# Optimization experiments

Hardware: AMD Instinct MI355X
Metric: run time of the kernel (lower is better)

Reference implementation:

```python
import jax, jax.numpy as jnp
import numpy as np

B, H, S, D = 4, 16, 2048, 64


def setup_inputs() -> dict:
    key = jax.random.key(0)
    kq, kk, kv = jax.random.split(key, 3)
    Q = jax.random.normal(kq, (B, H, S, D), dtype=jnp.float32)
    K = jax.random.normal(kk, (B, H, S, D), dtype=jnp.float32)
    V = jax.random.normal(kv, (B, H, S, D), dtype=jnp.float32)
    # causal mask, broadcasts over (B, H); True = keep, False (==0) = mask out
    mask = jnp.tril(jnp.ones((S, S), dtype=bool))
    return {"Q": Q, "K": K, "V": V, "mask": mask}


def reference(Q, K, V, mask):
    d_k = Q.shape[-1]
    scale = 1.0 / jnp.sqrt(jnp.asarray(d_k, dtype=Q.dtype))
    # [B,H,Sq,Sk] score matrix (the module materializes this fully)
    scores = jnp.einsum('bhqd,bhkd->bhqk', Q, K) * scale
    if mask is not None:
        scores = jnp.where(mask, scores, -jnp.inf)
    attn = jax.nn.softmax(scores, axis=-1)
    return jnp.einsum('bhqk,bhkd->bhqd', attn, V)
```

## Files before the change

kernel.cpp:

```cpp
#include <hip/hip_runtime.h>
#include <math.h>

namespace {

constexpr int SEQ   = 2048;
constexpr int DH    = 64;
constexpr int KVBLK = 64;
constexpr int BH    = 64;
constexpr size_t WS_NEED = (size_t)BH * SEQ * DH * 2  * 2 ;

typedef __bf16 bf16x8 __attribute__((ext_vector_type(8)));
typedef float  f32x16 __attribute__((ext_vector_type(16)));

union FragB { bf16x8 v; unsigned u[4]; };

__device__ __forceinline__ unsigned pack2(float a, float b) {
  unsigned r;
  asm("v_cvt_pk_bf16_f32 %0, %1, %2" : "=v"(r) : "v"(a), "v"(b));
  return r;
}

__device__ __forceinline__ unsigned short bf16c(float f) {
  union { float f; unsigned u; } v; v.f = f;
  unsigned r = v.u + 0x7fffu + ((v.u >> 16) & 1u);
  return (unsigned short)(r >> 16);
}

__device__ __forceinline__ void swap32(int a, int b, int &x, int &y) {
#if __has_builtin(__builtin_amdgcn_permlane32_swap)
  auto r = __builtin_amdgcn_permlane32_swap(a, b, false, false);
  x = r[0]; y = r[1];
#else
  const bool hi = ((threadIdx.x & 63) >= 32);
  const int sa = __shfl_xor(a, 32), sb = __shfl_xor(b, 32);
  x = hi ? sb : a;
  y = hi ? b  : sa;
#endif
}

__device__ __forceinline__ float xhalf_sum(float v) {
  int x, y; swap32(__float_as_int(v), __float_as_int(v), x, y);
  return __int_as_float(x) + __int_as_float(y);
}

__device__ __forceinline__ void gload16(const void* g, void* l) {
  __builtin_amdgcn_global_load_lds(
      (const __attribute__((address_space(1))) void*)g,
      (__attribute__((address_space(3))) void*)l, 16, 0, 0);
}

__global__ __launch_bounds__(256)
void prep(const float* __restrict__ Kg, const float* __restrict__ Vg,
          unsigned short* __restrict__ wsK, unsigned short* __restrict__ wsV)
{
  const int blk = blockIdx.x;
  const int bh  = blk & 63;
  const int t   = blk >> 6;
  const int tid = threadIdx.x;

  const float* Kb = Kg + (size_t)bh * SEQ * DH;
  unsigned short* wK = wsK + (size_t)bh * SEQ * DH;
#pragma unroll
  for (int i = 0; i < 2; ++i) {
    const int kc  = tid + i * 256;
    const int row = kc >> 3, c = kc & 7;
    const int csrc = c ^ (row & 7);
    const float* s = Kb + (size_t)(t*64 + row) * DH + csrc * 8;
    float4 a = *(const float4*)s, b2 = *(const float4*)(s + 4);
    uint4 w;
    w.x = pack2(a.x, a.y);   w.y = pack2(a.z, a.w);
    w.z = pack2(b2.x, b2.y); w.w = pack2(b2.z, b2.w);
    *(uint4*)&wK[(size_t)(t*64 + row) * DH + c * 8] = w;
  }

  __shared__ unsigned short vt[64 * 64];
  const float* Vb = Vg + (size_t)bh * SEQ * DH;
  {
    const int kv = tid >> 2;
    const int d0 = (tid & 3) * 16;
    const float* s = Vb + (size_t)(t*64 + kv) * DH + d0;
#pragma unroll
    for (int e = 0; e < 16; ++e) {
      const int d = d0 + e;
      const int slot = (kv >> 3) ^ (d & 7);
      vt[d*64 + slot*8 + (kv & 7)] = bf16c(s[e]);
    }
  }
  __syncthreads();
  unsigned short* wV = wsV + (size_t)bh * SEQ * DH + (size_t)t * 4096;
#pragma unroll
  for (int i = 0; i < 2; ++i) {
    const int o = (tid + i * 256) * 8;
    *(uint4*)&wV[o] = *(const uint4*)&vt[o];
  }
}

__global__ __launch_bounds__(256, 2)
void attn_fwd(const float* __restrict__ Qg, const unsigned short* __restrict__ wsK,
              const unsigned short* __restrict__ wsV, float* __restrict__ Og)
{
  const int b   = blockIdx.x;
  const int bh  = b & 63;
  const int qi  = 31 - (b >> 6);
  const int NT  = qi + 1;

  const int tid  = threadIdx.x;
  const int wv   = tid >> 6;
  const int rw   = wv & 1;
  const int kh   = wv >> 1;
  const int lane = tid & 63;
  const int l31  = lane & 31;
  const int hi   = lane >> 5;
  const int qloc = rw * 32 + l31;

  const float* Qp = Qg + (size_t)bh * SEQ * DH;
  const unsigned short* Kw = wsK + (size_t)bh * SEQ * DH;
  const unsigned short* Vw = wsV + (size_t)bh * SEQ * DH;
  float* Op = Og + (size_t)bh * SEQ * DH;

  __shared__ __align__(16) unsigned char smem[32768];

  const float qscale = 0.125f * 1.44269504088896f;
  FragB bq[4];
  {
    const float* src = Qp + (size_t)(qi*64 + rw*32 + l31) * DH + hi*8;
#pragma unroll
    for (int ks = 0; ks < 4; ++ks) {
      float4 f0 = *(const float4*)(src + ks*16);
      float4 f1 = *(const float4*)(src + ks*16 + 4);
      bq[ks].u[0] = pack2(f0.x*qscale, f0.y*qscale);
      bq[ks].u[1] = pack2(f0.z*qscale, f0.w*qscale);
      bq[ks].u[2] = pack2(f1.x*qscale, f1.y*qscale);
      bq[ks].u[3] = pack2(f1.z*qscale, f1.w*qscale);
    }
  }

  f32x16 oacc[2];
#pragma unroll
  for (int dt = 0; dt < 2; ++dt)
#pragma unroll
    for (int r = 0; r < 16; ++r) oacc[dt][r] = 0.f;
  float lpart = 0.f;

  auto stage = [&](int tile, int bufoff) {
    const unsigned short* gK = Kw + (size_t)tile * 4096 + wv*512 + lane*8;
    const unsigned short* gV = Vw + (size_t)tile * 4096 + wv*512 + lane*8;
    char* lb = (char*)smem + bufoff + wv*1024;
    gload16(gK,        lb);
    gload16(gK + 2048, lb + 4096);
    gload16(gV,        lb + 8192);
    gload16(gV + 2048, lb + 12288);
  };

  auto compute = [&](bool diag, int bufoff) {
    const unsigned short* Kl = (const unsigned short*)(smem + bufoff);
    const unsigned short* Vl = (const unsigned short*)(smem + bufoff + 8192);
    const int krow = kh*32 + l31;

    f32x16 st;
#pragma unroll
    for (int r = 0; r < 16; ++r) st[r] = 0.f;
    __builtin_amdgcn_s_setprio(1);
#pragma unroll
    for (int ks = 0; ks < 4; ++ks) {
      bf16x8 ak = *(const bf16x8*)&Kl[krow*64 + (((2*ks + hi) ^ (krow & 7)) * 8)];
      st = __builtin_amdgcn_mfma_f32_32x32x16_bf16(ak, bq[ks].v, st, 0, 0, 0);
    }
    __builtin_amdgcn_s_setprio(0);

    float p[16];
#pragma unroll
    for (int r = 0; r < 16; ++r) {
      float s = st[r];
      if (diag) {
        const int kvl = kh*32 + (r & 3) + 4*hi + 8*(r >> 2);
        if (kvl > qloc) s = -INFINITY;
      }
      const float e = exp2f(s);
      p[r] = e;
      lpart += e;
    }

    unsigned pk[8];
#pragma unroll
    for (int j2 = 0; j2 < 8; ++j2) pk[j2] = pack2(p[2*j2], p[2*j2 + 1]);

    FragB pa[2];
#pragma unroll
    for (int ks2 = 0; ks2 < 2; ++ks2) {
      const int gA = 2*ks2, gB = 2*ks2 + 1;
      int x0, y0, x1, y1;
      swap32((int)pk[2*gA],     (int)pk[2*gB],     x0, y0);
      swap32((int)pk[2*gA + 1], (int)pk[2*gB + 1], x1, y1);
      pa[ks2].u[0] = (unsigned)x0;
      pa[ks2].u[1] = (unsigned)x1;
      pa[ks2].u[2] = (unsigned)y0;
      pa[ks2].u[3] = (unsigned)y1;
    }

    __builtin_amdgcn_s_setprio(1);
#pragma unroll
    for (int dt = 0; dt < 2; ++dt) {
      const int d = dt*32 + l31;
#pragma unroll
      for (int ks2 = 0; ks2 < 2; ++ks2) {
        bf16x8 av = *(const bf16x8*)&Vl[d*64 + (((4*kh + 2*ks2 + hi) ^ (d & 7)) * 8)];
        oacc[dt] = __builtin_amdgcn_mfma_f32_32x32x16_bf16(av, pa[ks2].v, oacc[dt], 0, 0, 0);
      }
    }
    __builtin_amdgcn_s_setprio(0);
  };

  stage(0, 0);
  __syncthreads();

  for (int t = 0; t < NT; t += 2) {
    if (t + 1 < NT) stage(t + 1, 16384);
    compute(t == NT - 1, 0);
    __syncthreads();
    if (t + 1 < NT) {
      if (t + 2 < NT) stage(t + 2, 0);
      compute(t + 1 == NT - 1, 16384);
      __syncthreads();
    }
  }

  {
    float* reg0 = reinterpret_cast<float*>(smem);
    float* reg1 = reinterpret_cast<float*>(smem + 16384);
    float* myreg = rw ? reg1 : reg0;
    const int rb = l31 * 68;

    if (kh == 1) {
#pragma unroll
      for (int dt = 0; dt < 2; ++dt)
#pragma unroll
        for (int g4 = 0; g4 < 4; ++g4) {
          float4 w;
          w.x = oacc[dt][4*g4 + 0]; w.y = oacc[dt][4*g4 + 1];
          w.z = oacc[dt][4*g4 + 2]; w.w = oacc[dt][4*g4 + 3];
          *(float4*)&myreg[rb + dt*32 + 8*g4 + 4*hi] = w;
        }
      const float s1 = xhalf_sum(lpart);
      if (hi == 0) myreg[rb + 64] = s1;
    }
    __syncthreads();
    if (kh == 0) {
      const float linv = 1.0f / (xhalf_sum(lpart) + myreg[rb + 64]);
#pragma unroll
      for (int dt = 0; dt < 2; ++dt)
#pragma unroll
        for (int g4 = 0; g4 < 4; ++g4) {
          float4 v = *(const float4*)&myreg[rb + dt*32 + 8*g4 + 4*hi];
          v.x = (v.x + oacc[dt][4*g4 + 0]) * linv;
          v.y = (v.y + oacc[dt][4*g4 + 1]) * linv;
          v.z = (v.z + oacc[dt][4*g4 + 2]) * linv;
          v.w = (v.w + oacc[dt][4*g4 + 3]) * linv;
          *(float4*)&myreg[rb + dt*32 + 8*g4 + 4*hi] = v;
        }
    }
    __syncthreads();
    {
      float* dst = Op + (size_t)(qi * 64) * DH;
#pragma unroll
      for (int i = 0; i < 4; ++i) {
        const int f   = tid + i*256;
        const int row = f >> 4;
        const int ch  = f & 15;
        const float* srcrow = (row < 32) ? (reg0 + row*68) : (reg1 + (row-32)*68);
        float4 v = *(const float4*)&srcrow[ch*4];
        *(float4*)&dst[(size_t)row*DH + ch*4] = v;
      }
    }
  }
}

constexpr int PADB = 72;

__global__ __launch_bounds__(256, 2)
void attn_fb(const float* __restrict__ Qg, const float* __restrict__ Kg,
             const float* __restrict__ Vg, float* __restrict__ Og)
{
  const int b   = blockIdx.x;
  const int bh  = b & 63;
  const int qi  = 31 - (b >> 6);
  const int NT  = qi + 1;
  const int tid  = threadIdx.x;
  const int wv   = tid >> 6;
  const int rw   = wv & 1;
  const int kh   = wv >> 1;
  const int lane = tid & 63;
  const int l31  = lane & 31;
  const int hi   = lane >> 5;
  const int qloc = rw * 32 + l31;

  const size_t base = (size_t)bh * SEQ * DH;
  const float* Qp = Qg + base;
  const float* Kp = Kg + base;
  const float* Vp = Vg + base;
  float*       Op = Og + base;

  __shared__ __align__(16) unsigned char smem[18432];
  auto K_lds  = reinterpret_cast<__bf16(*)[PADB]>(smem);
  auto Vt_lds = reinterpret_cast<__bf16(*)[PADB]>(smem + 9216);

  const float qscale = 0.125f * 1.44269504088896f;
  FragB bq[4];
  {
    const float* src = Qp + (size_t)(qi*64 + rw*32 + l31) * DH + hi*8;
#pragma unroll
    for (int ks = 0; ks < 4; ++ks) {
      float4 f0 = *(const float4*)(src + ks*16);
      float4 f1 = *(const float4*)(src + ks*16 + 4);
      bq[ks].u[0] = pack2(f0.x*qscale, f0.y*qscale);
      bq[ks].u[1] = pack2(f0.z*qscale, f0.w*qscale);
      bq[ks].u[2] = pack2(f1.x*qscale, f1.y*qscale);
      bq[ks].u[3] = pack2(f1.z*qscale, f1.w*qscale);
    }
  }

  float4 kr[2][2];
  float  vr[16];
  const int kc8 = tid & 7;
  const int vd  = tid & 63;
  const int vk0 = (tid >> 6) * 16;

  auto load_tile = [&](int tile) {
    const int kvb = tile * KVBLK;
#pragma unroll
    for (int p = 0; p < 2; ++p) {
      const float* s = Kp + (size_t)(kvb + 32*p + (tid >> 3)) * DH + kc8*8;
      kr[p][0] = *(const float4*)s;
      kr[p][1] = *(const float4*)(s + 4);
    }
#pragma unroll
    for (int r = 0; r < 16; ++r)
      vr[r] = Vp[(size_t)(kvb + vk0 + r) * DH + vd];
  };

  auto store_tile = [&]() {
#pragma unroll
    for (int p = 0; p < 2; ++p) {
      uint4 w;
      w.x = pack2(kr[p][0].x, kr[p][0].y); w.y = pack2(kr[p][0].z, kr[p][0].w);
      w.z = pack2(kr[p][1].x, kr[p][1].y); w.w = pack2(kr[p][1].z, kr[p][1].w);
      *reinterpret_cast<uint4*>(&K_lds[32*p + (tid >> 3)][kc8*8]) = w;
    }
    uint4 w0, w1;
    w0.x = pack2(vr[0],  vr[1]);  w0.y = pack2(vr[2],  vr[3]);
    w0.z = pack2(vr[4],  vr[5]);  w0.w = pack2(vr[6],  vr[7]);
    w1.x = pack2(vr[8],  vr[9]);  w1.y = pack2(vr[10], vr[11]);
    w1.z = pack2(vr[12], vr[13]); w1.w = pack2(vr[14], vr[15]);
    *reinterpret_cast<uint4*>(&Vt_lds[vd][vk0])     = w0;
    *reinterpret_cast<uint4*>(&Vt_lds[vd][vk0 + 8]) = w1;
  };

  f32x16 oacc[2];
#pragma unroll
  for (int dt = 0; dt < 2; ++dt)
#pragma unroll
    for (int r = 0; r < 16; ++r) oacc[dt][r] = 0.f;
  float lpart = 0.f;

  load_tile(0);
  store_tile();
  __syncthreads();

  for (int t = 0; t < NT; ++t) {
    if (t + 1 < NT) load_tile(t + 1);
    const bool diag = (t == NT - 1);

    f32x16 st;
#pragma unroll
    for (int r = 0; r < 16; ++r) st[r] = 0.f;
#pragma unroll
    for (int ks = 0; ks < 4; ++ks) {
      bf16x8 ak = *(const bf16x8*)&K_lds[kh*32 + l31][ks*16 + hi*8];
      st = __builtin_amdgcn_mfma_f32_32x32x16_bf16(ak, bq[ks].v, st, 0, 0, 0);
    }

    float p[16];
#pragma unroll
    for (int r = 0; r < 16; ++r) {
      float s = st[r];
      if (diag) {
        const int kvl = kh*32 + (r & 3) + 4*hi + 8*(r >> 2);
        if (kvl > qloc) s = -INFINITY;
      }
      const float e = exp2f(s);
      p[r] = e;
      lpart += e;
    }

    unsigned pk[8];
#pragma unroll
    for (int j2 = 0; j2 < 8; ++j2) pk[j2] = pack2(p[2*j2], p[2*j2 + 1]);

    FragB pa[2];
#pragma unroll
    for (int ks2 = 0; ks2 < 2; ++ks2) {
      const int gA = 2*ks2, gB = 2*ks2 + 1;
      int x0, y0, x1, y1;
      swap32((int)pk[2*gA],     (int)pk[2*gB],     x0, y0);
      swap32((int)pk[2*gA + 1], (int)pk[2*gB + 1], x1, y1);
      pa[ks2].u[0] = (unsigned)x0;
      pa[ks2].u[1] = (unsigned)x1;
      pa[ks2].u[2] = (unsigned)y0;
      pa[ks2].u[3] = (unsigned)y1;
    }

#pragma unroll
    for (int dt = 0; dt < 2; ++dt)
#pragma unroll
      for (int ks2 = 0; ks2 < 2; ++ks2) {
        bf16x8 av = *(const bf16x8*)&Vt_lds[dt*32 + l31][kh*32 + ks2*16 + hi*8];
        oacc[dt] = __builtin_amdgcn_mfma_f32_32x32x16_bf16(av, pa[ks2].v, oacc[dt], 0, 0, 0);
      }

    __syncthreads();
    if (t + 1 < NT) {
      store_tile();
      __syncthreads();
    }
  }

  {
    float* reg0 = reinterpret_cast<float*>(smem);
    float* reg1 = reinterpret_cast<float*>(smem + 9216);
    float* myreg = rw ? reg1 : reg0;
    const int rb = l31 * 68;

    if (kh == 1) {
#pragma unroll
      for (int dt = 0; dt < 2; ++dt)
#pragma unroll
        for (int g4 = 0; g4 < 4; ++g4) {
          float4 w;
          w.x = oacc[dt][4*g4 + 0]; w.y = oacc[dt][4*g4 + 1];
          w.z = oacc[dt][4*g4 + 2]; w.w = oacc[dt][4*g4 + 3];
          *(float4*)&myreg[rb + dt*32 + 8*g4 + 4*hi] = w;
        }
      const float s1 = xhalf_sum(lpart);
      if (hi == 0) myreg[rb + 64] = s1;
    }
    __syncthreads();
    if (kh == 0) {
      const float linv = 1.0f / (xhalf_sum(lpart) + myreg[rb + 64]);
#pragma unroll
      for (int dt = 0; dt < 2; ++dt)
#pragma unroll
        for (int g4 = 0; g4 < 4; ++g4) {
          float4 v = *(const float4*)&myreg[rb + dt*32 + 8*g4 + 4*hi];
          v.x = (v.x + oacc[dt][4*g4 + 0]) * linv;
          v.y = (v.y + oacc[dt][4*g4 + 1]) * linv;
          v.z = (v.z + oacc[dt][4*g4 + 2]) * linv;
          v.w = (v.w + oacc[dt][4*g4 + 3]) * linv;
          *(float4*)&myreg[rb + dt*32 + 8*g4 + 4*hi] = v;
        }
    }
    __syncthreads();
    {
      float* dst = Op + (size_t)(qi * 64) * DH;
#pragma unroll
      for (int i = 0; i < 4; ++i) {
        const int f   = tid + i*256;
        const int row = f >> 4;
        const int ch  = f & 15;
        const float* srcrow = (row < 32) ? (reg0 + row*68) : (reg1 + (row-32)*68);
        float4 v = *(const float4*)&srcrow[ch*4];
        *(float4*)&dst[(size_t)row*DH + ch*4] = v;
      }
    }
  }
}

}

extern "C" void kernel_launch(void* const* d_in, const int* in_sizes, int n_in,
                              void* d_out, int out_size, void* d_ws, size_t ws_size,
                              hipStream_t stream) {
  const float* Q = (const float*)d_in[0];
  const float* K = (const float*)d_in[1];
  const float* V = (const float*)d_in[2];
  float* O = (float*)d_out;
  if (ws_size >= WS_NEED) {
    unsigned short* wsK = (unsigned short*)d_ws;
    unsigned short* wsV = wsK + (size_t)BH * SEQ * DH;
    prep<<<dim3(BH * 32), dim3(256), 0, stream>>>(K, V, wsK, wsV);
    attn_fwd<<<dim3(32 * BH), dim3(256), 0, stream>>>(Q, wsK, wsV, O);
  } else {
    attn_fb<<<dim3(32 * BH), dim3(256), 0, stream>>>(Q, K, V, O);
  }
}
```

Before: 81.23 us.

## Process 128-query tiles with 8 waves sharing each staged K/V tile

The attention kernel now uses 512-thread blocks that each handle 128 query rows, so every K/V tile staged into LDS is reused by four row-waves instead of two, halving the grid and the per-block global-to-LDS traffic per query. Waves covering the lower half of the query tile skip compute on the final KV tile they do not need. The epilogue reduces the two KV-half partial accumulators in two rounds and writes output directly from registers rather than through an LDS staging copy. The cost is larger blocks, with idle waves on the last tile and extra barriers, and direct global stores that may coalesce less well.

```diff
diff --git a/kernel.cpp b/kernel.cpp
--- a/kernel.cpp
+++ b/kernel.cpp
@@ -95,23 +95,24 @@
   }
 }
 
-__global__ __launch_bounds__(256, 2)
+__global__ __launch_bounds__(512, 4)
 void attn_fwd(const float* __restrict__ Qg, const unsigned short* __restrict__ wsK,
               const unsigned short* __restrict__ wsV, float* __restrict__ Og)
 {
   const int b   = blockIdx.x;
   const int bh  = b & 63;
-  const int qi  = 31 - (b >> 6);
-  const int NT  = qi + 1;
+  const int qi  = 15 - (b >> 6);
+  const int NT  = 2 * qi + 2;
 
   const int tid  = threadIdx.x;
   const int wv   = tid >> 6;
-  const int rw   = wv & 1;
-  const int kh   = wv >> 1;
+  const int rw   = wv & 3;
+  const int kh   = wv >> 2;
   const int lane = tid & 63;
   const int l31  = lane & 31;
   const int hi   = lane >> 5;
-  const int qloc = rw * 32 + l31;
+  const int qrel = (rw & 1) * 32 + l31;
+  const int tmaxw = 2*qi + (rw >> 1);
 
   const float* Qp = Qg + (size_t)bh * SEQ * DH;
   const unsigned short* Kw = wsK + (size_t)bh * SEQ * DH;
@@ -123,7 +124,7 @@
   const float qscale = 0.125f * 1.44269504088896f;
   FragB bq[4];
   {
-    const float* src = Qp + (size_t)(qi*64 + rw*32 + l31) * DH + hi*8;
+    const float* src = Qp + (size_t)(qi*128 + rw*32 + l31) * DH + hi*8;
 #pragma unroll
     for (int ks = 0; ks < 4; ++ks) {
       float4 f0 = *(const float4*)(src + ks*16);
@@ -146,10 +147,8 @@
     const unsigned short* gK = Kw + (size_t)tile * 4096 + wv*512 + lane*8;
     const unsigned short* gV = Vw + (size_t)tile * 4096 + wv*512 + lane*8;
     char* lb = (char*)smem + bufoff + wv*1024;
-    gload16(gK,        lb);
-    gload16(gK + 2048, lb + 4096);
-    gload16(gV,        lb + 8192);
-    gload16(gV + 2048, lb + 12288);
+    gload16(gK, lb);
+    gload16(gV, lb + 8192);
   };
 
   auto compute = [&](bool diag, int bufoff) {
@@ -174,7 +173,7 @@
       float s = st[r];
       if (diag) {
         const int kvl = kh*32 + (r & 3) + 4*hi + 8*(r >> 2);
-        if (kvl > qloc) s = -INFINITY;
+        if (kvl > qrel) s = -INFINITY;
       }
       const float e = exp2f(s);
       p[r] = e;
@@ -216,22 +215,22 @@
 
   for (int t = 0; t < NT; t += 2) {
     if (t + 1 < NT) stage(t + 1, 16384);
-    compute(t == NT - 1, 0);
+    if (t <= tmaxw) compute(t == tmaxw, 0);
     __syncthreads();
     if (t + 1 < NT) {
       if (t + 2 < NT) stage(t + 2, 0);
-      compute(t + 1 == NT - 1, 16384);
+      if (t + 1 <= tmaxw) compute(t + 1 == tmaxw, 16384);
       __syncthreads();
     }
   }
 
-  {
-    float* reg0 = reinterpret_cast<float*>(smem);
-    float* reg1 = reinterpret_cast<float*>(smem + 16384);
-    float* myreg = rw ? reg1 : reg0;
-    const int rb = l31 * 68;
-
-    if (kh == 1) {
+  const int qrow = qi*128 + rw*32 + l31;
+#pragma unroll
+  for (int round = 0; round < 2; ++round) {
+    __syncthreads();
+    if ((rw >> 1) == round && kh == 1) {
+      float* reg = reinterpret_cast<float*>(smem) + (rw & 1) * 4096;
+      const int rb = l31 * 65;
 #pragma unroll
       for (int dt = 0; dt < 2; ++dt)
 #pragma unroll
@@ -239,38 +238,28 @@
           float4 w;
           w.x = oacc[dt][4*g4 + 0]; w.y = oacc[dt][4*g4 + 1];
           w.z = oacc[dt][4*g4 + 2]; w.w = oacc[dt][4*g4 + 3];
-          *(float4*)&myreg[rb + dt*32 + 8*g4 + 4*hi] = w;
+          *(float4*)&reg[rb + dt*32 + 8*g4 + 4*hi] = w;
         }
       const float s1 = xhalf_sum(lpart);
-      if (hi == 0) myreg[rb + 64] = s1;
-    }
-    __syncthreads();
-    if (kh == 0) {
-      const float linv = 1.0f / (xhalf_sum(lpart) + myreg[rb + 64]);
+      if (hi == 0) reg[rb + 64] = s1;
+    }
+    __syncthreads();
+    if ((rw >> 1) == round && kh == 0) {
+      const float* reg = reinterpret_cast<const float*>(smem) + (rw & 1) * 4096;
+      const int rb = l31 * 65;
+      const float linv = 1.0f / (xhalf_sum(lpart) + reg[rb + 64]);
+      float* dst = Op + (size_t)qrow * DH;
 #pragma unroll
       for (int dt = 0; dt < 2; ++dt)
 #pragma unroll
         for (int g4 = 0; g4 < 4; ++g4) {
-          float4 v = *(const float4*)&myreg[rb + dt*32 + 8*g4 + 4*hi];
+          float4 v = *(const float4*)&reg[rb + dt*32 + 8*g4 + 4*hi];
           v.x = (v.x + oacc[dt][4*g4 + 0]) * linv;
           v.y = (v.y + oacc[dt][4*g4 + 1]) * linv;
           v.z = (v.z + oacc[dt][4*g4 + 2]) * linv;
           v.w = (v.w + oacc[dt][4*g4 + 3]) * linv;
-          *(float4*)&myreg[rb + dt*32 + 8*g4 + 4*hi] = v;
+          *(float4*)&dst[dt*32 + 8*g4 + 4*hi] = v;
         }
-    }
-    __syncthreads();
-    {
-      float* dst = Op + (size_t)(qi * 64) * DH;
-#pragma unroll
-      for (int i = 0; i < 4; ++i) {
-        const int f   = tid + i*256;
-        const int row = f >> 4;
-        const int ch  = f & 15;
-        const float* srcrow = (row < 32) ? (reg0 + row*68) : (reg1 + (row-32)*68);
-        float4 v = *(const float4*)&srcrow[ch*4];
-        *(float4*)&dst[(size_t)row*DH + ch*4] = v;
-      }
     }
   }
 }
@@ -487,7 +476,7 @@
     unsigned short* wsK = (unsigned short*)d_ws;
     unsigned short* wsV = wsK + (size_t)BH * SEQ * DH;
     prep<<<dim3(BH * 32), dim3(256), 0, stream>>>(K, V, wsK, wsV);
-    attn_fwd<<<dim3(32 * BH), dim3(256), 0, stream>>>(Q, wsK, wsV, O);
+    attn_fwd<<<dim3(16 * BH), dim3(512), 0, stream>>>(Q, wsK, wsV, O);
   } else {
     attn_fb<<<dim3(32 * BH), dim3(256), 0, stream>>>(Q, K, V, O);
   }
```

After: 83.51 us. 1.03x slower.

## Load K/V MFMA fragments directly from global into registers, drop LDS staging

Applied to the files above, without the earlier changes.

Removes the double-buffered LDS staging of K and V tiles (global_load_lds plus barriers) and instead has each wave load its MFMA operand fragments straight from global memory into registers, prefetching the next K tile while computing the current one. The prep kernel now writes an unswizzled K and V^T layout, with V transposed through a padded shared-memory array. LDS use in the main kernel shrinks to the epilogue reduction buffer, which may raise occupancy and removes per-tile barriers. The cost is that each wave pair sharing a kh reloads the same K/V data from global/L2 without reuse through LDS, and the V loads are no longer prefetched ahead of use.

```diff
diff --git a/kernel.cpp b/kernel.cpp
--- a/kernel.cpp
+++ b/kernel.cpp
@@ -43,12 +43,6 @@
   return __int_as_float(x) + __int_as_float(y);
 }
 
-__device__ __forceinline__ void gload16(const void* g, void* l) {
-  __builtin_amdgcn_global_load_lds(
-      (const __attribute__((address_space(1))) void*)g,
-      (__attribute__((address_space(3))) void*)l, 16, 0, 0);
-}
-
 __global__ __launch_bounds__(256)
 void prep(const float* __restrict__ Kg, const float* __restrict__ Vg,
           unsigned short* __restrict__ wsK, unsigned short* __restrict__ wsV)
@@ -64,8 +58,7 @@
   for (int i = 0; i < 2; ++i) {
     const int kc  = tid + i * 256;
     const int row = kc >> 3, c = kc & 7;
-    const int csrc = c ^ (row & 7);
-    const float* s = Kb + (size_t)(t*64 + row) * DH + csrc * 8;
+    const float* s = Kb + (size_t)(t*64 + row) * DH + c * 8;
     float4 a = *(const float4*)s, b2 = *(const float4*)(s + 4);
     uint4 w;
     w.x = pack2(a.x, a.y);   w.y = pack2(a.z, a.w);
@@ -73,25 +66,24 @@
     *(uint4*)&wK[(size_t)(t*64 + row) * DH + c * 8] = w;
   }
 
-  __shared__ unsigned short vt[64 * 64];
+  __shared__ unsigned short vt[64 * 72];
   const float* Vb = Vg + (size_t)bh * SEQ * DH;
   {
     const int kv = tid >> 2;
     const int d0 = (tid & 3) * 16;
     const float* s = Vb + (size_t)(t*64 + kv) * DH + d0;
 #pragma unroll
-    for (int e = 0; e < 16; ++e) {
-      const int d = d0 + e;
-      const int slot = (kv >> 3) ^ (d & 7);
-      vt[d*64 + slot*8 + (kv & 7)] = bf16c(s[e]);
-    }
+    for (int e = 0; e < 16; ++e)
+      vt[(d0 + e) * 72 + kv] = bf16c(s[e]);
   }
   __syncthreads();
   unsigned short* wV = wsV + (size_t)bh * SEQ * DH + (size_t)t * 4096;
 #pragma unroll
   for (int i = 0; i < 2; ++i) {
-    const int o = (tid + i * 256) * 8;
-    *(uint4*)&wV[o] = *(const uint4*)&vt[o];
+    const int idx = tid + i * 256;
+    const int d   = idx >> 3;
+    const int kvc = (idx & 7) * 8;
+    *(uint4*)&wV[d * 64 + kvc] = *(const uint4*)&vt[d * 72 + kvc];
   }
 }
 
@@ -118,7 +110,7 @@
   const unsigned short* Vw = wsV + (size_t)bh * SEQ * DH;
   float* Op = Og + (size_t)bh * SEQ * DH;
 
-  __shared__ __align__(16) unsigned char smem[32768];
+  __shared__ __align__(16) float sepi[2][32 * 68];
 
   const float qscale = 0.125f * 1.44269504088896f;
   FragB bq[4];
@@ -142,30 +134,35 @@
     for (int r = 0; r < 16; ++r) oacc[dt][r] = 0.f;
   float lpart = 0.f;
 
-  auto stage = [&](int tile, int bufoff) {
-    const unsigned short* gK = Kw + (size_t)tile * 4096 + wv*512 + lane*8;
-    const unsigned short* gV = Vw + (size_t)tile * 4096 + wv*512 + lane*8;
-    char* lb = (char*)smem + bufoff + wv*1024;
-    gload16(gK,        lb);
-    gload16(gK + 2048, lb + 4096);
-    gload16(gV,        lb + 8192);
-    gload16(gV + 2048, lb + 12288);
+  const unsigned short* Kbase = Kw + (size_t)(kh*32 + l31) * 64 + hi*8;
+  const unsigned short* Vb0   = Vw + (size_t)l31        * 64 + kh*32 + hi*8;
+  const unsigned short* Vb1   = Vw + (size_t)(32 + l31) * 64 + kh*32 + hi*8;
+
+  FragB ka[4], kb[4], vf[4];
+
+  auto loadK = [&](int t, FragB* k) {
+    const unsigned short* s = Kbase + (size_t)t * 4096;
+#pragma unroll
+    for (int ks = 0; ks < 4; ++ks) k[ks].v = *(const bf16x8*)(s + ks*16);
   };
-
-  auto compute = [&](bool diag, int bufoff) {
-    const unsigned short* Kl = (const unsigned short*)(smem + bufoff);
-    const unsigned short* Vl = (const unsigned short*)(smem + bufoff + 8192);
-    const int krow = kh*32 + l31;
-
+  auto loadV = [&](int t) {
+    const unsigned short* s0 = Vb0 + (size_t)t * 4096;
+    const unsigned short* s1 = Vb1 + (size_t)t * 4096;
+#pragma unroll
+    for (int ks2 = 0; ks2 < 2; ++ks2) {
+      vf[ks2].v     = *(const bf16x8*)(s0 + ks2*16);
+      vf[2 + ks2].v = *(const bf16x8*)(s1 + ks2*16);
+    }
+  };
+
+  auto compute = [&](const FragB* k, bool diag) {
     f32x16 st;
 #pragma unroll
     for (int r = 0; r < 16; ++r) st[r] = 0.f;
     __builtin_amdgcn_s_setprio(1);
 #pragma unroll
-    for (int ks = 0; ks < 4; ++ks) {
-      bf16x8 ak = *(const bf16x8*)&Kl[krow*64 + (((2*ks + hi) ^ (krow & 7)) * 8)];
-      st = __builtin_amdgcn_mfma_f32_32x32x16_bf16(ak, bq[ks].v, st, 0, 0, 0);
-    }
+    for (int ks = 0; ks < 4; ++ks)
+      st = __builtin_amdgcn_mfma_f32_32x32x16_bf16(k[ks].v, bq[ks].v, st, 0, 0, 0);
     __builtin_amdgcn_s_setprio(0);
 
     float p[16];
@@ -200,34 +197,29 @@
 
     __builtin_amdgcn_s_setprio(1);
 #pragma unroll
-    for (int dt = 0; dt < 2; ++dt) {
-      const int d = dt*32 + l31;
-#pragma unroll
-      for (int ks2 = 0; ks2 < 2; ++ks2) {
-        bf16x8 av = *(const bf16x8*)&Vl[d*64 + (((4*kh + 2*ks2 + hi) ^ (d & 7)) * 8)];
-        oacc[dt] = __builtin_amdgcn_mfma_f32_32x32x16_bf16(av, pa[ks2].v, oacc[dt], 0, 0, 0);
-      }
-    }
+    for (int dt = 0; dt < 2; ++dt)
+#pragma unroll
+      for (int ks2 = 0; ks2 < 2; ++ks2)
+        oacc[dt] = __builtin_amdgcn_mfma_f32_32x32x16_bf16(vf[2*dt + ks2].v, pa[ks2].v, oacc[dt], 0, 0, 0);
     __builtin_amdgcn_s_setprio(0);
   };
 
-  stage(0, 0);
-  __syncthreads();
-
-  for (int t = 0; t < NT; t += 2) {
-    if (t + 1 < NT) stage(t + 1, 16384);
-    compute(t == NT - 1, 0);
-    __syncthreads();
-    if (t + 1 < NT) {
-      if (t + 2 < NT) stage(t + 2, 0);
-      compute(t + 1 == NT - 1, 16384);
-      __syncthreads();
-    }
+  loadK(0, ka);
+  int t = 0;
+  while (true) {
+    loadV(t);
+    if (t + 1 < NT) loadK(t + 1, kb);
+    compute(ka, t == NT - 1);
+    if (++t >= NT) break;
+    loadV(t);
+    if (t + 1 < NT) loadK(t + 1, ka);
+    compute(kb, t == NT - 1);
+    if (++t >= NT) break;
   }
 
   {
-    float* reg0 = reinterpret_cast<float*>(smem);
-    float* reg1 = reinterpret_cast<float*>(smem + 16384);
+    float* reg0 = sepi[0];
+    float* reg1 = sepi[1];
     float* myreg = rw ? reg1 : reg0;
     const int rb = l31 * 68;
 
```

Measured after the change: 150.5 us. +85.3%, slower.

## Software-pipeline QK^T one tile ahead with split K/V staging buffers

Applied to the files above, without the earlier changes.

Splits K and V staging into separate rings, with triple-buffered K and double-buffered V, so the QK^T MFMA for the next tile is issued before softmax and PV of the current tile. The aim is to overlap exp and packing work with MFMA latency and to prefetch K two tiles ahead. It also splits the row-sum accumulator into two chains to shorten the dependency. In exchange it raises LDS use to 40KB and keeps an extra score fragment live in registers, which may reduce occupancy.

```diff
diff --git a/kernel.cpp b/kernel.cpp
--- a/kernel.cpp
+++ b/kernel.cpp
@@ -118,7 +118,7 @@
   const unsigned short* Vw = wsV + (size_t)bh * SEQ * DH;
   float* Op = Og + (size_t)bh * SEQ * DH;
 
-  __shared__ __align__(16) unsigned char smem[32768];
+  __shared__ __align__(16) unsigned char smem[40960];
 
   const float qscale = 0.125f * 1.44269504088896f;
   FragB bq[4];
@@ -140,23 +140,25 @@
   for (int dt = 0; dt < 2; ++dt)
 #pragma unroll
     for (int r = 0; r < 16; ++r) oacc[dt][r] = 0.f;
-  float lpart = 0.f;
-
-  auto stage = [&](int tile, int bufoff) {
+  float lp0 = 0.f, lp1 = 0.f;
+
+  auto stageK = [&](int tile) {
     const unsigned short* gK = Kw + (size_t)tile * 4096 + wv*512 + lane*8;
-    const unsigned short* gV = Vw + (size_t)tile * 4096 + wv*512 + lane*8;
-    char* lb = (char*)smem + bufoff + wv*1024;
+    char* lb = (char*)smem + (tile % 3) * 8192 + wv*1024;
     gload16(gK,        lb);
     gload16(gK + 2048, lb + 4096);
-    gload16(gV,        lb + 8192);
-    gload16(gV + 2048, lb + 12288);
   };
-
-  auto compute = [&](bool diag, int bufoff) {
-    const unsigned short* Kl = (const unsigned short*)(smem + bufoff);
-    const unsigned short* Vl = (const unsigned short*)(smem + bufoff + 8192);
-    const int krow = kh*32 + l31;
-
+  auto stageV = [&](int tile) {
+    const unsigned short* gV = Vw + (size_t)tile * 4096 + wv*512 + lane*8;
+    char* lb = (char*)smem + 24576 + (tile & 1) * 8192 + wv*1024;
+    gload16(gV,        lb);
+    gload16(gV + 2048, lb + 4096);
+  };
+
+  const int krow = kh*32 + l31;
+
+  auto qk = [&](int tile) -> f32x16 {
+    const unsigned short* Kl = (const unsigned short*)(smem + (tile % 3) * 8192);
     f32x16 st;
 #pragma unroll
     for (int r = 0; r < 16; ++r) st[r] = 0.f;
@@ -167,7 +169,10 @@
       st = __builtin_amdgcn_mfma_f32_32x32x16_bf16(ak, bq[ks].v, st, 0, 0, 0);
     }
     __builtin_amdgcn_s_setprio(0);
-
+    return st;
+  };
+
+  auto sm_pv = [&](const f32x16& st, int tile, bool diag) {
     float p[16];
 #pragma unroll
     for (int r = 0; r < 16; ++r) {
@@ -178,7 +183,7 @@
       }
       const float e = exp2f(s);
       p[r] = e;
-      lpart += e;
+      if (r & 1) lp1 += e; else lp0 += e;
     }
 
     unsigned pk[8];
@@ -198,6 +203,7 @@
       pa[ks2].u[3] = (unsigned)y1;
     }
 
+    const unsigned short* Vl = (const unsigned short*)(smem + 24576 + (tile & 1) * 8192);
     __builtin_amdgcn_s_setprio(1);
 #pragma unroll
     for (int dt = 0; dt < 2; ++dt) {
@@ -211,21 +217,29 @@
     __builtin_amdgcn_s_setprio(0);
   };
 
-  stage(0, 0);
+  stageK(0);
+  stageV(0);
+  if (NT > 1) stageK(1);
   __syncthreads();
+  f32x16 stA = qk(0), stB;
 
   for (int t = 0; t < NT; t += 2) {
-    if (t + 1 < NT) stage(t + 1, 16384);
-    compute(t == NT - 1, 0);
-    __syncthreads();
-    if (t + 1 < NT) {
-      if (t + 2 < NT) stage(t + 2, 0);
-      compute(t + 1 == NT - 1, 16384);
-      __syncthreads();
-    }
+    if (t + 2 < NT) stageK(t + 2);
+    if (t + 1 < NT) stageV(t + 1);
+    if (t + 1 < NT) stB = qk(t + 1);
+    sm_pv(stA, t, t == NT - 1);
+    __syncthreads();
+    if (t + 1 >= NT) break;
+
+    if (t + 3 < NT) stageK(t + 3);
+    if (t + 2 < NT) stageV(t + 2);
+    if (t + 2 < NT) stA = qk(t + 2);
+    sm_pv(stB, t + 1, t + 1 == NT - 1);
+    __syncthreads();
   }
 
   {
+    const float lpart = lp0 + lp1;
     float* reg0 = reinterpret_cast<float*>(smem);
     float* reg1 = reinterpret_cast<float*>(smem + 16384);
     float* myreg = rw ? reg1 : reg0;
```

Result: slower. 85.74 us (+5.5%).
